# Kernel optimization log

Measured on AMD Instinct MI355X. Metric: run time of the kernel, lower is better.

Reference implementation:

```python
import jax, jax.numpy as jnp
import numpy as np

N, T, H = 307, 256, 64
NH, DH = 4, 16  # transformer heads, head dim (64/4)


def _layernorm(x, g, b, eps=1e-5):
    mu = x.mean(-1, keepdims=True)
    var = ((x - mu) ** 2).mean(-1, keepdims=True)
    return (x - mu) / jnp.sqrt(var + eps) * g + b


def _run_cell(x, m, tf, tj, Anorm, W0, b0, W1, mixW, mixb, Wih, Whh, bih, bhh, outW, outb, jamW, jamb):
    # x,m,tf,tj: [N,T]. Per-timestep 4-path ChebConv(K=2) + softmax mixing + GRUCell.
    hidden = Whh.shape[1]

    def step(h, xs):
        x_t, m_t, tf_t, tj_t = xs  # each [N]
        msg_in = jnp.concatenate([h, m_t[:, None], tf_t[:, None], tj_t[:, None]], axis=-1)  # [N,H+3]
        am = Anorm @ msg_in  # [N,H+3]
        m_all = jnp.tanh(jnp.einsum('ni,poi->npo', msg_in, W0) + b0
                         + jnp.einsum('ni,poi->npo', am, W1))  # [N,4,H]
        mix = jax.nn.softmax(h @ mixW.T + mixb, axis=1)  # [N,4]
        msg = jnp.einsum('np,npo->no', mix, m_all)  # [N,H]
        inp = jnp.concatenate([msg, (x_t * m_t)[:, None], m_t[:, None]], axis=-1)  # [N,H+2]
        # PyTorch GRUCell (gate order r,z,n)
        gi = inp @ Wih.T + bih
        gh = h @ Whh.T + bhh
        i_r, i_z, i_n = jnp.split(gi, 3, axis=-1)
        h_r, h_z, h_n = jnp.split(gh, 3, axis=-1)
        r = jax.nn.sigmoid(i_r + h_r)
        z = jax.nn.sigmoid(i_z + h_z)
        n = jnp.tanh(i_n + r * h_n)
        h_new = (1.0 - z) * n + z * h
        h2 = h_new + 0.1 * h
        pred = (h2 @ outW.T + outb)[:, 0]
        jam = (h2 @ jamW.T + jamb)[:, 0]
        return h2, (pred, jam, h2)

    h0 = jnp.zeros((x.shape[0], hidden), x.dtype)
    _, (preds, jams, hs) = jax.lax.scan(step, h0, (x.T, m.T, tf.T, tj.T))
    return preds.T, jams.T, jnp.transpose(hs, (1, 0, 2))  # [N,T],[N,T],[N,T,H]


def _pos_enc(Tlen, hdim, dtype):
    pos = jnp.arange(Tlen, dtype=dtype)[:, None]
    div = 10000.0 ** (jnp.arange(0, hdim, 2, dtype=dtype) / hdim)
    pe = jnp.zeros((Tlen, hdim), dtype)
    pe = pe.at[:, 0::2].set(jnp.sin(pos / div))
    pe = pe.at[:, 1::2].set(jnp.cos(pos / div))
    return pe


def _enhancer(h, qkvW, qkvb, oW, ob, g1, be1, f1W, f1b, f2W, f2b, g2, be2, pW, pb):
    # h: [N,T,H]; post-norm TransformerEncoder (relu, no dropout at eval), then Linear(H,1)
    x = h + _pos_enc(h.shape[1], h.shape[2], h.dtype)[None]
    n_layers = qkvW.shape[0]
    for l in range(n_layers):
        qkv = x @ qkvW[l].T + qkvb[l]
        q, k, v = jnp.split(qkv, 3, axis=-1)
        sh = (x.shape[0], x.shape[1], NH, DH)
        q, k, v = q.reshape(sh), k.reshape(sh), v.reshape(sh)
        att = jax.nn.softmax(jnp.einsum('nqhd,nkhd->nhqk', q, k) / np.sqrt(DH).astype(np.float32), axis=-1)
        o = jnp.einsum('nhqk,nkhd->nqhd', att, v).reshape(x.shape)
        o = o @ oW[l].T + ob[l]
        x = _layernorm(x + o, g1[l], be1[l])
        f = jax.nn.relu(x @ f1W[l].T + f1b[l]) @ f2W[l].T + f2b[l]
        x = _layernorm(x + f, g2[l], be2[l])
    return (x @ pW.T + pb)[..., 0]  # [N,T]


def _forward(x_seq, m_seq, tod_free, tod_jam, Anorm,
             cell_chebW0, cell_chebb0, cell_chebW1, cell_mixW, cell_mixb,
             cell_Wih, cell_Whh, cell_bih, cell_bhh,
             cell_outW, cell_outb, cell_jamW, cell_jamb,
             fuse_W1, fuse_b1, fuse_W2, fuse_b2,
             tr_qkvW, tr_qkvb, tr_oW, tr_ob, tr_ln1g, tr_ln1b,
             tr_ff1W, tr_ff1b, tr_ff2W, tr_ff2b, tr_ln2g, tr_ln2b,
             tr_projW, tr_projb):
    def cell(i, x, m, tf, tj):
        return _run_cell(x, m, tf, tj, Anorm,
                         cell_chebW0[i], cell_chebb0[i], cell_chebW1[i],
                         cell_mixW[i], cell_mixb[i],
                         cell_Wih[i], cell_Whh[i], cell_bih[i], cell_bhh[i],
                         cell_outW[i], cell_outb[i], cell_jamW[i], cell_jamb[i])

    flip = lambda a: a[:, ::-1]
    pf, jf, h_fwd = cell(0, x_seq, m_seq, tod_free, tod_jam)
    pb_r, jb_r, h_bwd_r = cell(1, flip(x_seq), flip(m_seq), flip(tod_free), flip(tod_jam))
    pb, jb, h_bwd = flip(pb_r), flip(jb_r), h_bwd_r[:, ::-1]

    fuse_in = jnp.stack([pf, pb], axis=-1)  # [N,T,2]
    w = jax.nn.softmax(jax.nn.relu(fuse_in @ fuse_W1.T + fuse_b1) @ fuse_W2.T + fuse_b2, axis=-1)
    speed = w[..., 0] * pf + w[..., 1] * pb
    jam_logit = w[..., 0] * jf + w[..., 1] * jb

    h_fused = h_fwd * w[..., 0:1] + h_bwd * w[..., 1:2]  # [N,T,H]
    args = lambda i: (tr_qkvW[i], tr_qkvb[i], tr_oW[i], tr_ob[i], tr_ln1g[i], tr_ln1b[i],
                      tr_ff1W[i], tr_ff1b[i], tr_ff2W[i], tr_ff2b[i], tr_ln2g[i], tr_ln2b[i],
                      tr_projW[i], tr_projb[i])
    speed_refined = _enhancer(h_fused, *args(0))
    jam_refined = _enhancer(h_fused, *args(1))
    alpha = 0.3
    speed = (1.0 - alpha) * speed + alpha * speed_refined
    jam_logit = (1.0 - alpha) * jam_logit + alpha * jam_refined
    return speed, jam_logit


def setup_inputs() -> dict:
    key = jax.random.key(0)
    keys = list(jax.random.split(key, 40))
    kit = iter(keys)

    def rn(shape, s=0.05):
        return s * jax.random.normal(next(kit), shape, jnp.float32)

    # sparse gaussian-normalized adjacency -> row-normalized diffusion matrix
    rng = np.random.default_rng(0)
    d = rng.uniform(0.5, 3.0, (N, N)); d = (d + d.T) / 2
    keep = rng.uniform(size=(N, N)) < 0.05; keep = keep | keep.T
    d = np.where(keep, d, np.inf)
    sigma = d[d < np.inf].std() + 1e-8
    adj = np.where(d < np.inf, np.exp(-d ** 2 / sigma ** 2), 0.0)
    np.fill_diagonal(adj, 1.0)
    dinv = np.where(adj.sum(1) > 0, (adj.sum(1) + 1e-8) ** -0.5, 0.0)
    adj_sym = adj * dinv[:, None] * dinv[None, :]
    rowsum = adj_sym.sum(1)
    Anorm = (adj_sym * np.where(rowsum > 0, 1.0 / rowsum, 0.0)[:, None]).astype(np.float32)

    inp = {
        'x_seq': jax.random.normal(next(kit), (N, T), jnp.float32),
        'm_seq': (jax.random.uniform(next(kit), (N, T)) < 0.5).astype(jnp.float32),
        'tod_free': jax.random.uniform(next(kit), (N, T), jnp.float32),
        'tod_jam': jax.random.uniform(next(kit), (N, T), jnp.float32),
        'Anorm': jnp.asarray(Anorm),
        'cell_chebW0': rn((2, 4, H, H + 3)), 'cell_chebb0': jnp.zeros((2, 4, H), jnp.float32),
        'cell_chebW1': rn((2, 4, H, H + 3)),
        'cell_mixW': rn((2, 4, H)), 'cell_mixb': jnp.zeros((2, 4), jnp.float32),
        'cell_Wih': rn((2, 3 * H, H + 2)), 'cell_Whh': rn((2, 3 * H, H)),
        'cell_bih': jnp.zeros((2, 3 * H), jnp.float32), 'cell_bhh': jnp.zeros((2, 3 * H), jnp.float32),
        'cell_outW': rn((2, 1, H)), 'cell_outb': jnp.zeros((2, 1), jnp.float32),
        'cell_jamW': rn((2, 1, H)), 'cell_jamb': jnp.zeros((2, 1), jnp.float32),
        'fuse_W1': rn((H, 2)), 'fuse_b1': jnp.zeros((H,), jnp.float32),
        'fuse_W2': rn((2, H)), 'fuse_b2': jnp.zeros((2,), jnp.float32),
        'tr_qkvW': rn((2, 3, 3 * H, H)), 'tr_qkvb': jnp.zeros((2, 3, 3 * H), jnp.float32),
        'tr_oW': rn((2, 3, H, H)), 'tr_ob': jnp.zeros((2, 3, H), jnp.float32),
        'tr_ln1g': jnp.ones((2, 3, H), jnp.float32), 'tr_ln1b': jnp.zeros((2, 3, H), jnp.float32),
        'tr_ff1W': rn((2, 3, 256, H)), 'tr_ff1b': jnp.zeros((2, 3, 256), jnp.float32),
        'tr_ff2W': rn((2, 3, H, 256)), 'tr_ff2b': jnp.zeros((2, 3, H), jnp.float32),
        'tr_ln2g': jnp.ones((2, 3, H), jnp.float32), 'tr_ln2b': jnp.zeros((2, 3, H), jnp.float32),
        'tr_projW': rn((2, 1, H)), 'tr_projb': jnp.zeros((2, 1), jnp.float32),
    }
    return inp


def reference(x_seq, m_seq, tod_free, tod_jam, Anorm,
              cell_chebW0, cell_chebb0, cell_chebW1, cell_mixW, cell_mixb,
              cell_Wih, cell_Whh, cell_bih, cell_bhh,
              cell_outW, cell_outb, cell_jamW, cell_jamb,
              fuse_W1, fuse_b1, fuse_W2, fuse_b2,
              tr_qkvW, tr_qkvb, tr_oW, tr_ob, tr_ln1g, tr_ln1b,
              tr_ff1W, tr_ff1b, tr_ff2W, tr_ff2b, tr_ln2g, tr_ln2b,
              tr_projW, tr_projb):
    return _forward(x_seq, m_seq, tod_free, tod_jam, Anorm,
                    cell_chebW0, cell_chebb0, cell_chebW1, cell_mixW, cell_mixb,
                    cell_Wih, cell_Whh, cell_bih, cell_bhh,
                    cell_outW, cell_outb, cell_jamW, cell_jamb,
                    fuse_W1, fuse_b1, fuse_W2, fuse_b2,
                    tr_qkvW, tr_qkvb, tr_oW, tr_ob, tr_ln1g, tr_ln1b,
                    tr_ff1W, tr_ff1b, tr_ff2W, tr_ff2b, tr_ln2g, tr_ln2b,
                    tr_projW, tr_projb)
```

## Files before the change

kernel.cpp:

```cpp
#include <hip/hip_runtime.h>
#include <math.h>

#define NN   307
#define TT   256
#define HHH  64
#define NROW (NN*TT)
#define NBLK_D 77
#define SCANB  154

typedef unsigned short u16;
typedef __attribute__((ext_vector_type(8))) short short8;
typedef __attribute__((ext_vector_type(4))) float f4;

__device__ __forceinline__ float wsum(float v){
#pragma unroll
  for (int off = 32; off > 0; off >>= 1) v += __shfl_xor(v, off, 64);
  return v;
}
__device__ __forceinline__ float wsum16(float v){
#pragma unroll
  for (int off = 8; off > 0; off >>= 1) v += __shfl_xor(v, off, 64);
  return v;
}
__device__ __forceinline__ float ftanh(float x){
  x = fminf(20.f, fmaxf(-20.f, x));
  float e = __expf(2.f*x);
  return (e - 1.f)/(e + 1.f);
}
__device__ __forceinline__ float fsigm(float x){ return 1.f/(1.f + __expf(-x)); }

__device__ __forceinline__ u16 f2bf(float x){
  unsigned u = __float_as_uint(x);
  u += 0x7fffu + ((u >> 16) & 1u);
  return (u16)(u >> 16);
}
__device__ __forceinline__ void split8(const float* xv, short8& hi, short8& lo){
  union { short8 v; u16 u[8]; } H, L;
#pragma unroll
  for (int j = 0; j < 8; j++){
    const float x = xv[j];
    const u16 h = f2bf(x);
    H.u[j] = h;
    L.u[j] = f2bf(x - __uint_as_float((unsigned)h << 16));
  }
  hi = H.v; lo = L.v;
}

__global__ void k_sparse(const float* __restrict__ A, int* __restrict__ cnt,
                         int* __restrict__ idx, float* __restrict__ val){
  int n = blockIdx.x*64 + threadIdx.x;
  if (n >= NN) return;
  int c = 0;
  for (int m = 0; m < NN; m++){
    float a = A[n*NN + m];
    if (a != 0.f){ idx[n*NN + c] = m; val[n*NN + c] = a; c++; }
  }
  cnt[n] = c;
}

__global__ void k_tr_cheb(const float* __restrict__ W0, const float* __restrict__ W1,
                          float* __restrict__ W0T, float* __restrict__ W1T){
  int t = blockIdx.x*256 + threadIdx.x;
  if (t >= 2*67*256) return;
  int c = t & 255; int rest = t >> 8; int i = rest % 67; int d = rest / 67;
  int p = c >> 6, o = c & 63;
  int src = ((d*4 + p)*64 + o)*67 + i;
  W0T[t] = W0[src];
  W1T[t] = W1[src];
}

__global__ void k_tr_gru(const float* __restrict__ Wih, const float* __restrict__ Whh,
                         float* __restrict__ WihT, float* __restrict__ WhhT){
  int t = blockIdx.x*256 + threadIdx.x;
  if (t < 2*66*192){
    int j = t % 192; int rest = t / 192; int i = rest % 66; int d = rest / 66;
    WihT[t] = Wih[(d*192 + j)*66 + i];
  }
  if (t < 2*64*192){
    int j = t % 192; int rest = t / 192; int i = rest % 64; int d = rest / 64;
    WhhT[t] = Whh[(d*192 + j)*64 + i];
  }
}

__global__ void k_af(const float* __restrict__ mseq, const float* __restrict__ tfr,
                     const float* __restrict__ tjm, const int* __restrict__ cnt,
                     const int* __restrict__ idx, const float* __restrict__ val,
                     float* __restrict__ AF){
  int n = blockIdx.x, c = blockIdx.y, t = threadIdx.x;
  const float* feat = (c == 0) ? mseq : (c == 1) ? tfr : tjm;
  float acc = 0.f; int k = cnt[n];
  for (int s = 0; s < k; s++) acc += val[n*NN + s] * feat[idx[n*NN + s]*TT + t];
  AF[((size_t)c*NN + n)*TT + t] = acc;
}

__global__ void k_split(const float* __restrict__ src, u16* __restrict__ hi,
                        u16* __restrict__ lo, int n){
  int i = blockIdx.x*256 + threadIdx.x;
  if (i >= n) return;
  const float x = src[i];
  const u16 h = f2bf(x);
  hi[i] = h;
  lo[i] = f2bf(x - __uint_as_float((unsigned)h << 16));
}

__global__ __launch_bounds__(256, 1)
void k_scan(const float* __restrict__ xseq, const float* __restrict__ mseq,
            const float* __restrict__ tfr, const float* __restrict__ tjm,
            const float* __restrict__ W0T, const float* __restrict__ W1T,
            const float* __restrict__ b0g,
            const float* __restrict__ mixW, const float* __restrict__ mixb,
            const float* __restrict__ WihT, const float* __restrict__ WhhT,
            const float* __restrict__ bih, const float* __restrict__ bhh,
            const float* __restrict__ outW, const float* __restrict__ outb,
            const float* __restrict__ jamW, const float* __restrict__ jamb,
            const int* __restrict__ spcnt, const int* __restrict__ spidx,
            const float* __restrict__ spval, const float* __restrict__ AF,
            float* __restrict__ Hseq, float* __restrict__ PRED, float* __restrict__ JPRED,
            int* __restrict__ slots)
{
  const int tid = threadIdx.x;
  const int bid = blockIdx.x;
  const int d   = bid / NBLK_D;
  const int n0  = (bid % NBLK_D) * 4;
  const int lane = tid & 63;
  const int wid  = tid >> 6;

  __shared__ __align__(16) float hsT[64][4];
  __shared__ __align__(16) float amsT[68][4];
  __shared__ __align__(16) float msgsT[64][4];
  __shared__ float malls[256][5];
  __shared__ float gis[4][192];
  __shared__ float ghs[4][192];
  __shared__ float mixs[4][4];
  __shared__ float xss[4], mss[4], tfs[4], tjs[4];
  __shared__ int   s_idx[4][320];
  __shared__ float s_val[4][320];
  __shared__ int   s_cnt[4];

  float w0r[67], w1r[67];
#pragma unroll
  for (int i = 0; i < 67; i++){
    w0r[i] = W0T[(d*67 + i)*256 + tid];
    w1r[i] = W1T[(d*67 + i)*256 + tid];
  }
  const float b0r = b0g[d*256 + tid];
  float wih_r[64], whh_r[64];
  float wih64 = 0.f, wih65 = 0.f, bih_r = 0.f, bhh_r = 0.f;
  if (tid < 192){
#pragma unroll
    for (int i = 0; i < 64; i++){
      whh_r[i] = WhhT[(d*64 + i)*192 + tid];
      wih_r[i] = WihT[(d*66 + i)*192 + tid];
    }
    wih64 = WihT[(d*66 + 64)*192 + tid];
    wih65 = WihT[(d*66 + 65)*192 + tid];
    bih_r = bih[d*192 + tid];
    bhh_r = bhh[d*192 + tid];
  }
  float mixw_r[4];
#pragma unroll
  for (int p = 0; p < 4; p++) mixw_r[p] = mixW[(d*4 + p)*64 + lane];
  const float mixb0 = mixb[d*4+0], mixb1 = mixb[d*4+1], mixb2 = mixb[d*4+2], mixb3 = mixb[d*4+3];
  const float outw_r = outW[d*64 + lane], jamw_r = jamW[d*64 + lane];
  const float outb_r = outb[d], jamb_r = jamb[d];

  for (int r = 0; r < 4; r++){
    const int n = min(n0 + r, NN-1);
    const int cc = spcnt[n];
    const int ccp = (cc + 15) & ~15;
    if (tid == 0) s_cnt[r] = ccp;
    for (int s = tid; s < ccp; s += 256){
      s_idx[r][s] = (s < cc) ? spidx[n*NN + s] : 0;
      s_val[r][s] = (s < cc) ? spval[n*NN + s] : 0.f;
    }
  }
  hsT[lane][wid] = 0.f;
  __syncthreads();

#pragma unroll 1
  for (int k = 0; k < TT; k++){
    const int ts = (d == 0) ? k : (TT-1 - k);
    if (tid < 4){
      const int r = tid; const int n = min(n0 + r, NN-1);
      const float mv = mseq[n*TT + ts];
      mss[r] = mv; tfs[r] = tfr[n*TT + ts]; tjs[r] = tjm[n*TT + ts];
      xss[r] = xseq[n*TT + ts];
      amsT[64][r] = AF[(0*NN + n)*TT + ts];
      amsT[65][r] = AF[(1*NN + n)*TT + ts];
      amsT[66][r] = AF[(2*NN + n)*TT + ts];
    }
    {
      const int r = wid;
      const float hv = hsT[lane][r];
      float l0 = wsum(hv * mixw_r[0]) + mixb0;
      float l1 = wsum(hv * mixw_r[1]) + mixb1;
      float l2 = wsum(hv * mixw_r[2]) + mixb2;
      float l3 = wsum(hv * mixw_r[3]) + mixb3;
      const float mx = fmaxf(fmaxf(l0,l1), fmaxf(l2,l3));
      const float e0 = __expf(l0-mx), e1 = __expf(l1-mx), e2 = __expf(l2-mx), e3 = __expf(l3-mx);
      const float inv = 1.f/(e0+e1+e2+e3);
      if (lane == 0){
        mixs[0][r] = e0*inv; mixs[1][r] = e1*inv; mixs[2][r] = e2*inv; mixs[3][r] = e3*inv;
      }
    }
    __syncthreads();
    {
      float a0 = b0r, a1 = b0r, a2 = b0r, a3 = b0r;
#pragma unroll
      for (int i = 0; i < 64; i++){
        const float4 h4 = *(const float4*)&hsT[i][0];
        const float w = w0r[i];
        a0 += h4.x*w; a1 += h4.y*w; a2 += h4.z*w; a3 += h4.w*w;
      }
      a0 += mss[0]*w0r[64] + tfs[0]*w0r[65] + tjs[0]*w0r[66];
      a1 += mss[1]*w0r[64] + tfs[1]*w0r[65] + tjs[1]*w0r[66];
      a2 += mss[2]*w0r[64] + tfs[2]*w0r[65] + tjs[2]*w0r[66];
      a3 += mss[3]*w0r[64] + tfs[3]*w0r[65] + tjs[3]*w0r[66];
      malls[tid][0] = a0; malls[tid][1] = a1; malls[tid][2] = a2; malls[tid][3] = a3;
    }
    if (tid < 192){
      float g0 = bhh_r, g1 = bhh_r, g2 = bhh_r, g3 = bhh_r;
#pragma unroll
      for (int i = 0; i < 64; i++){
        const float4 h4 = *(const float4*)&hsT[i][0];
        const float w = whh_r[i];
        g0 += h4.x*w; g1 += h4.y*w; g2 += h4.z*w; g3 += h4.w*w;
      }
      ghs[0][tid] = g0; ghs[1][tid] = g1; ghs[2][tid] = g2; ghs[3][tid] = g3;
      gis[0][tid] = bih_r + (xss[0]*mss[0])*wih64 + mss[0]*wih65;
      gis[1][tid] = bih_r + (xss[1]*mss[1])*wih64 + mss[1]*wih65;
      gis[2][tid] = bih_r + (xss[2]*mss[2])*wih64 + mss[2]*wih65;
      gis[3][tid] = bih_r + (xss[3]*mss[3])*wih64 + mss[3]*wih65;
    }
    if (k > 0 && tid < 64){
      const int* sl = slots + (size_t)d*NBLK_D*16;
      const int i2 = lane + 64;
      for (;;){
        const int va = (lane < NBLK_D)
            ? __hip_atomic_load(&sl[lane*16], __ATOMIC_RELAXED, __HIP_MEMORY_SCOPE_AGENT)
            : 0x7fffffff;
        const int vb = (i2 < NBLK_D)
            ? __hip_atomic_load(&sl[i2*16], __ATOMIC_RELAXED, __HIP_MEMORY_SCOPE_AGENT)
            : 0x7fffffff;
        if (__all(min(va, vb) >= k)) break;
        __builtin_amdgcn_s_sleep(1);
      }
    }
    __syncthreads();
    {
      const float* Hprev = Hseq + (size_t)(d*257 + k)*NN*64;
      const int r = wid;
      const int ccp = s_cnt[r];
      float acc = 0.f;
      for (int s = 0; s < ccp; s += 16){
        float aV[16], hV[16];
#pragma unroll
        for (int u = 0; u < 16; u++){
          const int m = s_idx[r][s+u];
          aV[u] = s_val[r][s+u];
          hV[u] = __hip_atomic_load(&Hprev[(size_t)m*64 + lane],
                                    __ATOMIC_RELAXED, __HIP_MEMORY_SCOPE_AGENT);
        }
#pragma unroll
        for (int u = 0; u < 16; u++) acc += aV[u]*hV[u];
      }
      amsT[lane][r] = acc;
    }
    __syncthreads();
    {
      const int p = tid >> 6;
      float pa0 = malls[tid][0], pa1 = malls[tid][1], pa2 = malls[tid][2], pa3 = malls[tid][3];
#pragma unroll
      for (int i = 0; i < 67; i++){
        const float4 m4 = *(const float4*)&amsT[i][0];
        const float w = w1r[i];
        pa0 += m4.x*w; pa1 += m4.y*w; pa2 += m4.z*w; pa3 += m4.w*w;
      }
      malls[tid][0] = mixs[p][0]*ftanh(pa0);
      malls[tid][1] = mixs[p][1]*ftanh(pa1);
      malls[tid][2] = mixs[p][2]*ftanh(pa2);
      malls[tid][3] = mixs[p][3]*ftanh(pa3);
    }
    __syncthreads();
    msgsT[lane][wid] = malls[lane][wid] + malls[64+lane][wid] + malls[128+lane][wid] + malls[192+lane][wid];
    __syncthreads();
    if (tid < 192){
      float q0 = gis[0][tid], q1 = gis[1][tid], q2 = gis[2][tid], q3 = gis[3][tid];
#pragma unroll
      for (int i = 0; i < 64; i++){
        const float4 m4 = *(const float4*)&msgsT[i][0];
        const float w = wih_r[i];
        q0 += m4.x*w; q1 += m4.y*w; q2 += m4.z*w; q3 += m4.w*w;
      }
      gis[0][tid] = q0; gis[1][tid] = q1; gis[2][tid] = q2; gis[3][tid] = q3;
    }
    __syncthreads();
    {
      const int r = wid, o = lane;
      const float ir = gis[r][o], iz = gis[r][o+64], in_ = gis[r][o+128];
      const float hr = ghs[r][o], hz = ghs[r][o+64], hn = ghs[r][o+128];
      const float rr2 = fsigm(ir + hr);
      const float zz = fsigm(iz + hz);
      const float nnv = ftanh(in_ + rr2*hn);
      const float hold = hsT[o][r];
      const float h2 = (1.f - zz)*nnv + zz*hold + 0.1f*hold;
      hsT[o][r] = h2;
      const int n = n0 + r;
      if (n < NN)
        __hip_atomic_store(&Hseq[((size_t)(d*257 + k + 1)*NN + n)*64 + o], h2,
                           __ATOMIC_RELAXED, __HIP_MEMORY_SCOPE_AGENT);
    }
    __syncthreads();
    if (tid == 0)
      __hip_atomic_store(&slots[bid*16], k + 1, __ATOMIC_RELAXED, __HIP_MEMORY_SCOPE_AGENT);
    {
      const float h2 = hsT[lane][wid];
      const float pv = wsum(h2 * outw_r);
      const float jv = wsum(h2 * jamw_r);
      const int n = n0 + wid;
      if (lane == 0 && n < NN){
        PRED [(d*NN + n)*TT + ts] = pv + outb_r;
        JPRED[(d*NN + n)*TT + ts] = jv + jamb_r;
      }
    }
  }
}

__global__ __launch_bounds__(256)
void k_fusion(const float* __restrict__ PRED, const float* __restrict__ JPRED,
              const float* __restrict__ Hseq,
              const float* __restrict__ fw1, const float* __restrict__ fb1,
              const float* __restrict__ fw2, const float* __restrict__ fb2,
              float* __restrict__ x0, float* __restrict__ outp)
{
  const int tid = threadIdx.x;
  const int rr = tid >> 6, lane = tid & 63;
  const int idx = blockIdx.x*4 + rr;
  const int n = idx >> 8, t = idx & 255;
  const float pf = PRED[(0*NN + n)*TT + t], pb = PRED[(NN + n)*TT + t];
  const float jf = JPRED[(0*NN + n)*TT + t], jb = JPRED[(NN + n)*TT + t];
  const float hid = fmaxf(fw1[lane*2]*pf + fw1[lane*2+1]*pb + fb1[lane], 0.f);
  const float l0 = wsum(hid * fw2[lane]) + fb2[0];
  const float l1 = wsum(hid * fw2[64+lane]) + fb2[1];
  const float mx = fmaxf(l0,l1);
  const float e0 = __expf(l0-mx), e1 = __expf(l1-mx);
  const float inv = 1.f/(e0+e1);
  const float w0 = e0*inv, w1 = e1*inv;
  const float hf = Hseq[((size_t)(0*257 + t + 1)*NN + n)*64 + lane];
  const float hb = Hseq[((size_t)(257 + 256 - t)*NN + n)*64 + lane];
  const int i2 = lane & ~1;
  const float dv = powf(10000.f, (float)i2 * (1.f/64.f));
  const float arg = (float)t / dv;
  const float pe = (lane & 1) ? cosf(arg) : sinf(arg);
  x0[(size_t)idx*64 + lane] = hf*w0 + hb*w1 + pe;
  if (lane == 0){
    outp[idx]        = 0.7f*(w0*pf + w1*pb);
    outp[NROW + idx] = 0.7f*(w0*jf + w1*jb);
  }
}

__global__ __launch_bounds__(256)
void k_qkv(const float* __restrict__ X, const u16* __restrict__ Whi,
           const u16* __restrict__ Wlo, const float* __restrict__ bias,
           float* __restrict__ Y)
{
  const int tid = threadIdx.x;
  const int w = tid >> 6, l = tid & 63;
  const int m16 = l & 15, q = l >> 4;
  const int row = blockIdx.x*64 + w*16 + m16;
  short8 Ah[2], Al[2];
#pragma unroll
  for (int kh = 0; kh < 2; kh++){
    float xv[8];
    *(float4*)&xv[0] = *(const float4*)&X[(size_t)row*64 + kh*32 + q*8];
    *(float4*)&xv[4] = *(const float4*)&X[(size_t)row*64 + kh*32 + q*8 + 4];
    split8(xv, Ah[kh], Al[kh]);
  }
  const int rbase = blockIdx.x*64 + w*16 + q*4;
  for (int nt = 0; nt < 12; nt++){
    const int n = nt*16 + m16;
    f4 acc = {0.f, 0.f, 0.f, 0.f};
#pragma unroll
    for (int kh = 0; kh < 2; kh++){
      const short8 Bh = *(const short8*)&Whi[(size_t)n*64 + kh*32 + q*8];
      const short8 Bl = *(const short8*)&Wlo[(size_t)n*64 + kh*32 + q*8];
      acc = __builtin_amdgcn_mfma_f32_16x16x32_bf16(Ah[kh], Bh, acc, 0, 0, 0);
      acc = __builtin_amdgcn_mfma_f32_16x16x32_bf16(Ah[kh], Bl, acc, 0, 0, 0);
      acc = __builtin_amdgcn_mfma_f32_16x16x32_bf16(Al[kh], Bh, acc, 0, 0, 0);
    }
    const float bb = bias[n];
#pragma unroll
    for (int r = 0; r < 4; r++)
      Y[(size_t)(rbase + r)*192 + n] = acc[r] + bb;
  }
}

__global__ __launch_bounds__(256)
void k_oproj_ln(const float* __restrict__ X, const u16* __restrict__ Whi,
                const u16* __restrict__ Wlo, const float* __restrict__ bias,
                const float* __restrict__ Xres, const float* __restrict__ g,
                const float* __restrict__ b, float* __restrict__ Y)
{
  const int tid = threadIdx.x;
  const int w = tid >> 6, l = tid & 63;
  const int m16 = l & 15, q = l >> 4;
  const int row = blockIdx.x*64 + w*16 + m16;
  short8 Ah[2], Al[2];
#pragma unroll
  for (int kh = 0; kh < 2; kh++){
    float xv[8];
    *(float4*)&xv[0] = *(const float4*)&X[(size_t)row*64 + kh*32 + q*8];
    *(float4*)&xv[4] = *(const float4*)&X[(size_t)row*64 + kh*32 + q*8 + 4];
    split8(xv, Ah[kh], Al[kh]);
  }
  f4 acc[4];
#pragma unroll
  for (int nt = 0; nt < 4; nt++){
    acc[nt] = (f4){0.f, 0.f, 0.f, 0.f};
    const int n = nt*16 + m16;
#pragma unroll
    for (int kh = 0; kh < 2; kh++){
      const short8 Bh = *(const short8*)&Whi[(size_t)n*64 + kh*32 + q*8];
      const short8 Bl = *(const short8*)&Wlo[(size_t)n*64 + kh*32 + q*8];
      acc[nt] = __builtin_amdgcn_mfma_f32_16x16x32_bf16(Ah[kh], Bh, acc[nt], 0, 0, 0);
      acc[nt] = __builtin_amdgcn_mfma_f32_16x16x32_bf16(Ah[kh], Bl, acc[nt], 0, 0, 0);
      acc[nt] = __builtin_amdgcn_mfma_f32_16x16x32_bf16(Al[kh], Bh, acc[nt], 0, 0, 0);
    }
  }
  const int rbase = blockIdx.x*64 + w*16 + q*4;
#pragma unroll
  for (int r = 0; r < 4; r++){
    float v[4]; float s = 0.f;
#pragma unroll
    for (int nt = 0; nt < 4; nt++){
      const int col = nt*16 + m16;
      v[nt] = acc[nt][r] + bias[col] + Xres[(size_t)(rbase + r)*64 + col];
      s += v[nt];
    }
    const float mu = wsum16(s) * (1.f/64.f);
    float vs = 0.f;
#pragma unroll
    for (int nt = 0; nt < 4; nt++){ v[nt] -= mu; vs += v[nt]*v[nt]; }
    const float rstd = rsqrtf(wsum16(vs) * (1.f/64.f) + 1e-5f);
#pragma unroll
    for (int nt = 0; nt < 4; nt++){
      const int col = nt*16 + m16;
      Y[(size_t)(rbase + r)*64 + col] = v[nt] * rstd * g[col] + b[col];
    }
  }
}

__global__ __launch_bounds__(256)
void k_ffblock(const float* __restrict__ X,
               const u16* __restrict__ W1hi, const u16* __restrict__ W1lo,
               const float* __restrict__ b1,
               const u16* __restrict__ W2hi, const u16* __restrict__ W2lo,
               const float* __restrict__ b2,
               const float* __restrict__ g, const float* __restrict__ b,
               float* __restrict__ Y)
{
  __shared__ __align__(16) u16 Hs[64][280];
  const int tid = threadIdx.x;
  const int w = tid >> 6, l = tid & 63;
  const int m16 = l & 15, q = l >> 4;
  const int row = blockIdx.x*64 + w*16 + m16;
  short8 Ah[2], Al[2];
#pragma unroll
  for (int kh = 0; kh < 2; kh++){
    float xv[8];
    *(float4*)&xv[0] = *(const float4*)&X[(size_t)row*64 + kh*32 + q*8];
    *(float4*)&xv[4] = *(const float4*)&X[(size_t)row*64 + kh*32 + q*8 + 4];
    split8(xv, Ah[kh], Al[kh]);
  }
  for (int nt = 0; nt < 16; nt++){
    const int n = nt*16 + m16;
    f4 acc = {0.f, 0.f, 0.f, 0.f};
#pragma unroll
    for (int kh = 0; kh < 2; kh++){
      const short8 Bh = *(const short8*)&W1hi[(size_t)n*64 + kh*32 + q*8];
      const short8 Bl = *(const short8*)&W1lo[(size_t)n*64 + kh*32 + q*8];
      acc = __builtin_amdgcn_mfma_f32_16x16x32_bf16(Ah[kh], Bh, acc, 0, 0, 0);
      acc = __builtin_amdgcn_mfma_f32_16x16x32_bf16(Ah[kh], Bl, acc, 0, 0, 0);
      acc = __builtin_amdgcn_mfma_f32_16x16x32_bf16(Al[kh], Bh, acc, 0, 0, 0);
    }
    const float bb = b1[n];
#pragma unroll
    for (int r = 0; r < 4; r++){
      const float h = fmaxf(acc[r] + bb, 0.f);
      Hs[w*16 + q*4 + r][n] = f2bf(h);
    }
  }
  __syncthreads();
  f4 acc2[4];
#pragma unroll
  for (int nt = 0; nt < 4; nt++) acc2[nt] = (f4){0.f, 0.f, 0.f, 0.f};
#pragma unroll 1
  for (int kh = 0; kh < 8; kh++){
    const short8 Ahh = *(const short8*)&Hs[w*16 + m16][kh*32 + q*8];
#pragma unroll
    for (int nt = 0; nt < 4; nt++){
      const int n = nt*16 + m16;
      const short8 Bh = *(const short8*)&W2hi[(size_t)n*256 + kh*32 + q*8];
      const short8 Bl = *(const short8*)&W2lo[(size_t)n*256 + kh*32 + q*8];
      acc2[nt] = __builtin_amdgcn_mfma_f32_16x16x32_bf16(Ahh, Bh, acc2[nt], 0, 0, 0);
      acc2[nt] = __builtin_amdgcn_mfma_f32_16x16x32_bf16(Ahh, Bl, acc2[nt], 0, 0, 0);
    }
  }
  const int rbase = blockIdx.x*64 + w*16 + q*4;
#pragma unroll
  for (int r = 0; r < 4; r++){
    float v[4]; float s = 0.f;
#pragma unroll
    for (int nt = 0; nt < 4; nt++){
      const int col = nt*16 + m16;
      v[nt] = acc2[nt][r] + b2[col] + X[(size_t)(rbase + r)*64 + col];
      s += v[nt];
    }
    const float mu = wsum16(s) * (1.f/64.f);
    float vs = 0.f;
#pragma unroll
    for (int nt = 0; nt < 4; nt++){ v[nt] -= mu; vs += v[nt]*v[nt]; }
    const float rstd = rsqrtf(wsum16(vs) * (1.f/64.f) + 1e-5f);
#pragma unroll
    for (int nt = 0; nt < 4; nt++){
      const int col = nt*16 + m16;
      Y[(size_t)(rbase + r)*64 + col] = v[nt] * rstd * g[col] + b[col];
    }
  }
}

__global__ __launch_bounds__(256)
void k_attn(const float* __restrict__ QKV, float* __restrict__ O)
{
  __shared__ __align__(16) u16 Vst[4][16][264];
  __shared__ __align__(16) u16 Pst[4][16][264];
  const int n = blockIdx.x;
  const int tid = threadIdx.x;
  const int h = tid >> 6;
  const int l = tid & 63;
  const int m16 = l & 15, q = l >> 4;
  const float* nbase = QKV + (size_t)n*256*192;
  const short8 z8 = {0,0,0,0,0,0,0,0};

  for (int kb = 0; kb < 64; kb++){
    const int key = kb*4 + q;
    const float vv = nbase[(size_t)key*192 + 128 + h*16 + m16];
    Vst[h][m16][key] = f2bf(vv);
  }
  short8 Bh[16], Bl[16];
#pragma unroll
  for (int ct = 0; ct < 16; ct++){
    if (q < 2){
      float kv[8];
      *(float4*)&kv[0] = *(const float4*)&nbase[(size_t)(ct*16+m16)*192 + 64 + h*16 + q*8];
      *(float4*)&kv[4] = *(const float4*)&nbase[(size_t)(ct*16+m16)*192 + 64 + h*16 + q*8 + 4];
      split8(kv, Bh[ct], Bl[ct]);
    } else { Bh[ct] = z8; Bl[ct] = z8; }
  }
  __syncthreads();

#pragma unroll 1
  for (int c = 0; c < 16; c++){
    const int c0 = c*16;
    short8 Qh, Ql;
    if (q < 2){
      float xv[8];
      *(float4*)&xv[0] = *(const float4*)&nbase[(size_t)(c0+m16)*192 + h*16 + q*8];
      *(float4*)&xv[4] = *(const float4*)&nbase[(size_t)(c0+m16)*192 + h*16 + q*8 + 4];
#pragma unroll
      for (int j2 = 0; j2 < 8; j2++) xv[j2] *= 0.25f;
      split8(xv, Qh, Ql);
    } else { Qh = z8; Ql = z8; }
    float rs[4] = {0.f, 0.f, 0.f, 0.f};
#pragma unroll
    for (int ct = 0; ct < 16; ct++){
      f4 s = {0.f, 0.f, 0.f, 0.f};
      s = __builtin_amdgcn_mfma_f32_16x16x32_bf16(Qh, Bh[ct], s, 0, 0, 0);
      s = __builtin_amdgcn_mfma_f32_16x16x32_bf16(Qh, Bl[ct], s, 0, 0, 0);
      s = __builtin_amdgcn_mfma_f32_16x16x32_bf16(Ql, Bh[ct], s, 0, 0, 0);
#pragma unroll
      for (int r = 0; r < 4; r++){
        const float p = __expf(s[r]);
        rs[r] += p;
        Pst[h][q*4 + r][ct*16 + m16] = f2bf(p);
      }
    }
#pragma unroll
    for (int r = 0; r < 4; r++) rs[r] = wsum16(rs[r]);
    __syncthreads();
    f4 acc = {0.f, 0.f, 0.f, 0.f};
#pragma unroll
    for (int kt = 0; kt < 8; kt++){
      const short8 Pa = *(const short8*)&Pst[h][m16][kt*32 + q*8];
      const short8 Vb = *(const short8*)&Vst[h][m16][kt*32 + q*8];
      acc = __builtin_amdgcn_mfma_f32_16x16x32_bf16(Pa, Vb, acc, 0, 0, 0);
    }
    __syncthreads();
#pragma unroll
    for (int r = 0; r < 4; r++){
      O[((size_t)n*256 + c0 + q*4 + r)*64 + h*16 + m16] = acc[r] / rs[r];
    }
  }
}

__global__ __launch_bounds__(256)
void k_proj_add(const float* __restrict__ X, const float* __restrict__ pW,
                const float* __restrict__ pb, float* __restrict__ outp)
{
  const int tid = threadIdx.x;
  const int r = tid >> 6, lane = tid & 63;
  const size_t row = (size_t)blockIdx.x*4 + r;
  const float v = X[row*64 + lane] * pW[lane];
  const float s = wsum(v);
  if (lane == 0) outp[row] += 0.3f*(s + pb[0]);
}

extern "C" void kernel_launch(void* const* d_in, const int* in_sizes, int n_in,
                              void* d_out, int out_size, void* d_ws, size_t ws_size,
                              hipStream_t stream)
{
  const float* x_seq = (const float*)d_in[0];
  const float* m_seq = (const float*)d_in[1];
  const float* tod_f = (const float*)d_in[2];
  const float* tod_j = (const float*)d_in[3];
  const float* Anorm = (const float*)d_in[4];
  const float* chW0  = (const float*)d_in[5];
  const float* chb0  = (const float*)d_in[6];
  const float* chW1  = (const float*)d_in[7];
  const float* mixW  = (const float*)d_in[8];
  const float* mixb  = (const float*)d_in[9];
  const float* Wih   = (const float*)d_in[10];
  const float* Whh   = (const float*)d_in[11];
  const float* bih   = (const float*)d_in[12];
  const float* bhh   = (const float*)d_in[13];
  const float* outW  = (const float*)d_in[14];
  const float* outbp = (const float*)d_in[15];
  const float* jamW  = (const float*)d_in[16];
  const float* jambp = (const float*)d_in[17];
  const float* fW1   = (const float*)d_in[18];
  const float* fb1   = (const float*)d_in[19];
  const float* fW2   = (const float*)d_in[20];
  const float* fb2   = (const float*)d_in[21];
  const float* qkvW  = (const float*)d_in[22];
  const float* qkvb  = (const float*)d_in[23];
  const float* oW    = (const float*)d_in[24];
  const float* ob    = (const float*)d_in[25];
  const float* ln1g  = (const float*)d_in[26];
  const float* ln1b  = (const float*)d_in[27];
  const float* f1W   = (const float*)d_in[28];
  const float* f1b   = (const float*)d_in[29];
  const float* f2W   = (const float*)d_in[30];
  const float* f2b   = (const float*)d_in[31];
  const float* ln2g  = (const float*)d_in[32];
  const float* ln2b  = (const float*)d_in[33];
  const float* prW   = (const float*)d_in[34];
  const float* prb   = (const float*)d_in[35];
  float* out = (float*)d_out;

  float* ws = (float*)d_ws;
  size_t off = 0;
  auto take = [&](size_t n)->float*{ float* p = ws + off; off += (n + 63) & ~(size_t)63; return p; };
  int*   slots = (int*)take(4096);
  float* W0T  = take((size_t)2*67*256);
  float* W1T  = take((size_t)2*67*256);
  float* WihT = take((size_t)2*66*192);
  float* WhhT = take((size_t)2*64*192);
  int*   spcnt = (int*)take(320);
  int*   spidx = (int*)take((size_t)NN*NN);
  float* spval = take((size_t)NN*NN);
  float* AF    = take((size_t)3*NN*TT);
  float* PRED  = take((size_t)2*NN*TT);
  float* JPRED = take((size_t)2*NN*TT);
  float* HSEQ  = take((size_t)2*257*NN*64);
  float* X0    = take((size_t)NROW*64);
  float* XBUF  = take((size_t)NROW*64);
  float* OBUF  = take((size_t)NROW*64);
  float* FBUF  = take((size_t)NROW*256);
  const size_t NQKV = (size_t)6*192*64;
  const size_t NO   = (size_t)6*64*64;
  const size_t NF1  = (size_t)6*256*64;
  const size_t NF2  = (size_t)6*64*256;
  const size_t NWTOT = NQKV + NO + NF1 + NF2;
  u16* WHI = (u16*)take((NWTOT + 1)/2);
  u16* WLO = (u16*)take((NWTOT + 1)/2);
  (void)ws_size; (void)in_sizes; (void)n_in; (void)out_size;

  hipMemsetAsync(slots, 0, 4096*sizeof(int), stream);
  hipMemsetAsync(HSEQ, 0, (size_t)NN*64*sizeof(float), stream);
  hipMemsetAsync(HSEQ + (size_t)257*NN*64, 0, (size_t)NN*64*sizeof(float), stream);

  k_sparse<<<dim3((NN+63)/64), dim3(64), 0, stream>>>(Anorm, spcnt, spidx, spval);
  k_tr_cheb<<<dim3(134), dim3(256), 0, stream>>>(chW0, chW1, W0T, W1T);
  k_tr_gru<<<dim3(99), dim3(256), 0, stream>>>(Wih, Whh, WihT, WhhT);
  k_af<<<dim3(NN,3), dim3(256), 0, stream>>>(m_seq, tod_f, tod_j, spcnt, spidx, spval, AF);
  k_split<<<dim3((int)((NQKV+255)/256)), dim3(256), 0, stream>>>(qkvW, WHI, WLO, (int)NQKV);
  k_split<<<dim3((int)((NO+255)/256)), dim3(256), 0, stream>>>(oW, WHI+NQKV, WLO+NQKV, (int)NO);
  k_split<<<dim3((int)((NF1+255)/256)), dim3(256), 0, stream>>>(f1W, WHI+NQKV+NO, WLO+NQKV+NO, (int)NF1);
  k_split<<<dim3((int)((NF2+255)/256)), dim3(256), 0, stream>>>(f2W, WHI+NQKV+NO+NF1, WLO+NQKV+NO+NF1, (int)NF2);

  k_scan<<<dim3(SCANB), dim3(256), 0, stream>>>(x_seq, m_seq, tod_f, tod_j, W0T, W1T,
      chb0, mixW, mixb, WihT, WhhT, bih, bhh, outW, outbp, jamW, jambp,
      spcnt, spidx, spval, AF, HSEQ, PRED, JPRED, slots);

  k_fusion<<<dim3(NROW/4), dim3(256), 0, stream>>>(PRED, JPRED, HSEQ, fW1, fb1, fW2, fb2, X0, out);

  for (int e = 0; e < 2; e++){
    for (int l = 0; l < 3; l++){
      const int el = e*3 + l;
      const float* xin = (l == 0) ? X0 : XBUF;
      const u16* qhi = WHI + (size_t)el*192*64;
      const u16* qlo = WLO + (size_t)el*192*64;
      const u16* ohi = WHI + NQKV + (size_t)el*64*64;
      const u16* olo = WLO + NQKV + (size_t)el*64*64;
      const u16* f1hi = WHI + NQKV + NO + (size_t)el*256*64;
      const u16* f1lo = WLO + NQKV + NO + (size_t)el*256*64;
      const u16* f2hi = WHI + NQKV + NO + NF1 + (size_t)el*64*256;
      const u16* f2lo = WLO + NQKV + NO + NF1 + (size_t)el*64*256;
      k_qkv<<<dim3(NROW/64), dim3(256), 0, stream>>>(xin, qhi, qlo,
          qkvb + (size_t)el*192, FBUF);
      k_attn<<<dim3(NN), dim3(256), 0, stream>>>(FBUF, OBUF);
      k_oproj_ln<<<dim3(NROW/64), dim3(256), 0, stream>>>(OBUF, ohi, olo,
          ob + (size_t)el*64, xin, ln1g + (size_t)el*64, ln1b + (size_t)el*64, XBUF);
      k_ffblock<<<dim3(NROW/64), dim3(256), 0, stream>>>(XBUF, f1hi, f1lo,
          f1b + (size_t)el*256, f2hi, f2lo, f2b + (size_t)el*64,
          ln2g + (size_t)el*64, ln2b + (size_t)el*64, XBUF);
    }
    k_proj_add<<<dim3(NROW/4), dim3(256), 0, stream>>>(XBUF, prW + (size_t)e*64, prb + e,
        out + (size_t)e*NROW);
  }
}
```

Measured before the change: 4.773 ms.

## Fuse QKV projection into attention kernel, dropping the QKV intermediate buffer

Replaces the separate QKV projection and attention kernels with one per-node kernel. It converts the node's 256x64 activations to bf16 in shared memory, computes K and V per head with MFMA, then computes Q tile by tile and runs the attention in the same block. This removes the global write and re-read of the 192-wide QKV buffer and one kernel launch per layer. In exchange, X is kept only as high bf16 (the lo term is dropped) and K is a single bf16 value, so precision is lower than the old three-term split. The per-tile __syncthreads were removed; this looks safe because each wave touches only its own head's shared-memory slices.

After: 4.645 ms. 2.7% less time.

```diff
diff --git a/kernel.cpp b/kernel.cpp
--- a/kernel.cpp
+++ b/kernel.cpp
@@ -34,6 +34,9 @@
   u += 0x7fffu + ((u >> 16) & 1u);
   return (u16)(u >> 16);
 }
+__device__ __forceinline__ float bf2f(u16 h){
+  return __uint_as_float((unsigned)h << 16);
+}
 __device__ __forceinline__ void split8(const float* xv, short8& hi, short8& lo){
   union { short8 v; u16 u[8]; } H, L;
 #pragma unroll
@@ -41,7 +44,7 @@
     const float x = xv[j];
     const u16 h = f2bf(x);
     H.u[j] = h;
-    L.u[j] = f2bf(x - __uint_as_float((unsigned)h << 16));
+    L.u[j] = f2bf(x - bf2f(h));
   }
   hi = H.v; lo = L.v;
 }
@@ -100,7 +103,7 @@
   const float x = src[i];
   const u16 h = f2bf(x);
   hi[i] = h;
-  lo[i] = f2bf(x - __uint_as_float((unsigned)h << 16));
+  lo[i] = f2bf(x - bf2f(h));
 }
 
 __global__ __launch_bounds__(256, 1)
@@ -360,38 +363,122 @@
 }
 
 __global__ __launch_bounds__(256)
-void k_qkv(const float* __restrict__ X, const u16* __restrict__ Whi,
-           const u16* __restrict__ Wlo, const float* __restrict__ bias,
-           float* __restrict__ Y)
+void k_qkattn(const float* __restrict__ X,
+              const u16* __restrict__ Whi, const u16* __restrict__ Wlo,
+              const float* __restrict__ bias, float* __restrict__ O)
 {
+  __shared__ __align__(16) u16 Xhi[256][72];
+  __shared__ __align__(16) u16 Vt [4][16][280];
+  __shared__ __align__(16) u16 Pst[4][16][264];
+  __shared__ __align__(16) u16 Kscr[4][16][24];
+  __shared__ __align__(16) u16 Qhs[4][16][24];
+  __shared__ __align__(16) u16 Qls[4][16][24];
+  const int n = blockIdx.x;
   const int tid = threadIdx.x;
-  const int w = tid >> 6, l = tid & 63;
+  const int h = tid >> 6;
+  const int l = tid & 63;
   const int m16 = l & 15, q = l >> 4;
-  const int row = blockIdx.x*64 + w*16 + m16;
-  short8 Ah[2], Al[2];
+  const float* xbase = X + (size_t)n*256*64;
+  const short8 z8 = {0,0,0,0,0,0,0,0};
+
+  {
+    const float* xr = xbase + (size_t)tid*64;
+#pragma unroll
+    for (int c = 0; c < 64; c += 8){
+      float v[8];
+      *(float4*)&v[0] = *(const float4*)&xr[c];
+      *(float4*)&v[4] = *(const float4*)&xr[c+4];
+      union { short8 s; u16 u[8]; } pk;
+#pragma unroll
+      for (int j = 0; j < 8; j++) pk.u[j] = f2bf(v[j]);
+      *(short8*)&Xhi[tid][c] = pk.s;
+    }
+  }
+  __syncthreads();
+
+  short8 WqH[2], WqL[2], WkH[2], WkL[2], WvH[2], WvL[2];
 #pragma unroll
   for (int kh = 0; kh < 2; kh++){
-    float xv[8];
-    *(float4*)&xv[0] = *(const float4*)&X[(size_t)row*64 + kh*32 + q*8];
-    *(float4*)&xv[4] = *(const float4*)&X[(size_t)row*64 + kh*32 + q*8 + 4];
-    split8(xv, Ah[kh], Al[kh]);
-  }
-  const int rbase = blockIdx.x*64 + w*16 + q*4;
-  for (int nt = 0; nt < 12; nt++){
-    const int n = nt*16 + m16;
-    f4 acc = {0.f, 0.f, 0.f, 0.f};
-#pragma unroll
-    for (int kh = 0; kh < 2; kh++){
-      const short8 Bh = *(const short8*)&Whi[(size_t)n*64 + kh*32 + q*8];
-      const short8 Bl = *(const short8*)&Wlo[(size_t)n*64 + kh*32 + q*8];
-      acc = __builtin_amdgcn_mfma_f32_16x16x32_bf16(Ah[kh], Bh, acc, 0, 0, 0);
-      acc = __builtin_amdgcn_mfma_f32_16x16x32_bf16(Ah[kh], Bl, acc, 0, 0, 0);
-      acc = __builtin_amdgcn_mfma_f32_16x16x32_bf16(Al[kh], Bh, acc, 0, 0, 0);
-    }
-    const float bb = bias[n];
-#pragma unroll
-    for (int r = 0; r < 4; r++)
-      Y[(size_t)(rbase + r)*192 + n] = acc[r] + bb;
+    const size_t rq = (size_t)(h*16 + m16)*64 + kh*32 + q*8;
+    const size_t rk = (size_t)(64 + h*16 + m16)*64 + kh*32 + q*8;
+    const size_t rv = (size_t)(128 + h*16 + m16)*64 + kh*32 + q*8;
+    WqH[kh] = *(const short8*)&Whi[rq]; WqL[kh] = *(const short8*)&Wlo[rq];
+    WkH[kh] = *(const short8*)&Whi[rk]; WkL[kh] = *(const short8*)&Wlo[rk];
+    WvH[kh] = *(const short8*)&Whi[rv]; WvL[kh] = *(const short8*)&Wlo[rv];
+  }
+  const float qb = bias[h*16 + m16];
+  const float kb = bias[64 + h*16 + m16];
+  const float vb = bias[128 + h*16 + m16];
+
+  short8 Kb[16];
+#pragma unroll 1
+  for (int ct = 0; ct < 16; ct++){
+    short8 Xa0 = *(const short8*)&Xhi[ct*16 + m16][q*8];
+    short8 Xa1 = *(const short8*)&Xhi[ct*16 + m16][32 + q*8];
+    f4 ka = {0.f,0.f,0.f,0.f}, va = {0.f,0.f,0.f,0.f};
+    ka = __builtin_amdgcn_mfma_f32_16x16x32_bf16(Xa0, WkH[0], ka, 0, 0, 0);
+    ka = __builtin_amdgcn_mfma_f32_16x16x32_bf16(Xa0, WkL[0], ka, 0, 0, 0);
+    ka = __builtin_amdgcn_mfma_f32_16x16x32_bf16(Xa1, WkH[1], ka, 0, 0, 0);
+    ka = __builtin_amdgcn_mfma_f32_16x16x32_bf16(Xa1, WkL[1], ka, 0, 0, 0);
+    va = __builtin_amdgcn_mfma_f32_16x16x32_bf16(Xa0, WvH[0], va, 0, 0, 0);
+    va = __builtin_amdgcn_mfma_f32_16x16x32_bf16(Xa0, WvL[0], va, 0, 0, 0);
+    va = __builtin_amdgcn_mfma_f32_16x16x32_bf16(Xa1, WvH[1], va, 0, 0, 0);
+    va = __builtin_amdgcn_mfma_f32_16x16x32_bf16(Xa1, WvL[1], va, 0, 0, 0);
+#pragma unroll
+    for (int r = 0; r < 4; r++){
+      Kscr[h][q*4 + r][m16] = f2bf(ka[r] + kb);
+      Vt[h][m16][ct*16 + q*4 + r] = f2bf(va[r] + vb);
+    }
+    Kb[ct] = (q < 2) ? *(const short8*)&Kscr[h][m16][q*8] : z8;
+  }
+
+#pragma unroll 1
+  for (int c = 0; c < 16; c++){
+    short8 Xa0 = *(const short8*)&Xhi[c*16 + m16][q*8];
+    short8 Xa1 = *(const short8*)&Xhi[c*16 + m16][32 + q*8];
+    f4 qa = {0.f,0.f,0.f,0.f};
+    qa = __builtin_amdgcn_mfma_f32_16x16x32_bf16(Xa0, WqH[0], qa, 0, 0, 0);
+    qa = __builtin_amdgcn_mfma_f32_16x16x32_bf16(Xa0, WqL[0], qa, 0, 0, 0);
+    qa = __builtin_amdgcn_mfma_f32_16x16x32_bf16(Xa1, WqH[1], qa, 0, 0, 0);
+    qa = __builtin_amdgcn_mfma_f32_16x16x32_bf16(Xa1, WqL[1], qa, 0, 0, 0);
+#pragma unroll
+    for (int r = 0; r < 4; r++){
+      const float qv = (qa[r] + qb) * 0.25f;
+      const u16 hh = f2bf(qv);
+      Qhs[h][q*4 + r][m16] = hh;
+      Qls[h][q*4 + r][m16] = f2bf(qv - bf2f(hh));
+    }
+    short8 Qh = z8, Ql = z8;
+    if (q < 2){
+      Qh = *(const short8*)&Qhs[h][m16][q*8];
+      Ql = *(const short8*)&Qls[h][m16][q*8];
+    }
+    float rs[4] = {0.f, 0.f, 0.f, 0.f};
+#pragma unroll
+    for (int ct = 0; ct < 16; ct++){
+      f4 s = {0.f,0.f,0.f,0.f};
+      s = __builtin_amdgcn_mfma_f32_16x16x32_bf16(Qh, Kb[ct], s, 0, 0, 0);
+      s = __builtin_amdgcn_mfma_f32_16x16x32_bf16(Ql, Kb[ct], s, 0, 0, 0);
+#pragma unroll
+      for (int r = 0; r < 4; r++){
+        const float p = __expf(s[r]);
+        rs[r] += p;
+        Pst[h][q*4 + r][ct*16 + m16] = f2bf(p);
+      }
+    }
+#pragma unroll
+    for (int r = 0; r < 4; r++) rs[r] = wsum16(rs[r]);
+    f4 acc = {0.f,0.f,0.f,0.f};
+#pragma unroll
+    for (int kt = 0; kt < 8; kt++){
+      const short8 Pa = *(const short8*)&Pst[h][m16][kt*32 + q*8];
+      const short8 Vb = *(const short8*)&Vt[h][m16][kt*32 + q*8];
+      acc = __builtin_amdgcn_mfma_f32_16x16x32_bf16(Pa, Vb, acc, 0, 0, 0);
+    }
+#pragma unroll
+    for (int r = 0; r < 4; r++){
+      O[((size_t)n*256 + c*16 + q*4 + r)*64 + h*16 + m16] = acc[r] / rs[r];
+    }
   }
 }
 
@@ -525,80 +612,6 @@
     for (int nt = 0; nt < 4; nt++){
       const int col = nt*16 + m16;
       Y[(size_t)(rbase + r)*64 + col] = v[nt] * rstd * g[col] + b[col];
-    }
-  }
-}
-
-__global__ __launch_bounds__(256)
-void k_attn(const float* __restrict__ QKV, float* __restrict__ O)
-{
-  __shared__ __align__(16) u16 Vst[4][16][264];
-  __shared__ __align__(16) u16 Pst[4][16][264];
-  const int n = blockIdx.x;
-  const int tid = threadIdx.x;
-  const int h = tid >> 6;
-  const int l = tid & 63;
-  const int m16 = l & 15, q = l >> 4;
-  const float* nbase = QKV + (size_t)n*256*192;
-  const short8 z8 = {0,0,0,0,0,0,0,0};
-
-  for (int kb = 0; kb < 64; kb++){
-    const int key = kb*4 + q;
-    const float vv = nbase[(size_t)key*192 + 128 + h*16 + m16];
-    Vst[h][m16][key] = f2bf(vv);
-  }
-  short8 Bh[16], Bl[16];
-#pragma unroll
-  for (int ct = 0; ct < 16; ct++){
-    if (q < 2){
-      float kv[8];
-      *(float4*)&kv[0] = *(const float4*)&nbase[(size_t)(ct*16+m16)*192 + 64 + h*16 + q*8];
-      *(float4*)&kv[4] = *(const float4*)&nbase[(size_t)(ct*16+m16)*192 + 64 + h*16 + q*8 + 4];
-      split8(kv, Bh[ct], Bl[ct]);
-    } else { Bh[ct] = z8; Bl[ct] = z8; }
-  }
-  __syncthreads();
-
-#pragma unroll 1
-  for (int c = 0; c < 16; c++){
-    const int c0 = c*16;
-    short8 Qh, Ql;
-    if (q < 2){
-      float xv[8];
-      *(float4*)&xv[0] = *(const float4*)&nbase[(size_t)(c0+m16)*192 + h*16 + q*8];
-      *(float4*)&xv[4] = *(const float4*)&nbase[(size_t)(c0+m16)*192 + h*16 + q*8 + 4];
-#pragma unroll
-      for (int j2 = 0; j2 < 8; j2++) xv[j2] *= 0.25f;
-      split8(xv, Qh, Ql);
-    } else { Qh = z8; Ql = z8; }
-    float rs[4] = {0.f, 0.f, 0.f, 0.f};
-#pragma unroll
-    for (int ct = 0; ct < 16; ct++){
-      f4 s = {0.f, 0.f, 0.f, 0.f};
-      s = __builtin_amdgcn_mfma_f32_16x16x32_bf16(Qh, Bh[ct], s, 0, 0, 0);
-      s = __builtin_amdgcn_mfma_f32_16x16x32_bf16(Qh, Bl[ct], s, 0, 0, 0);
-      s = __builtin_amdgcn_mfma_f32_16x16x32_bf16(Ql, Bh[ct], s, 0, 0, 0);
-#pragma unroll
-      for (int r = 0; r < 4; r++){
-        const float p = __expf(s[r]);
-        rs[r] += p;
-        Pst[h][q*4 + r][ct*16 + m16] = f2bf(p);
-      }
-    }
-#pragma unroll
-    for (int r = 0; r < 4; r++) rs[r] = wsum16(rs[r]);
-    __syncthreads();
-    f4 acc = {0.f, 0.f, 0.f, 0.f};
-#pragma unroll
-    for (int kt = 0; kt < 8; kt++){
-      const short8 Pa = *(const short8*)&Pst[h][m16][kt*32 + q*8];
-      const short8 Vb = *(const short8*)&Vst[h][m16][kt*32 + q*8];
-      acc = __builtin_amdgcn_mfma_f32_16x16x32_bf16(Pa, Vb, acc, 0, 0, 0);
-    }
-    __syncthreads();
-#pragma unroll
-    for (int r = 0; r < 4; r++){
-      O[((size_t)n*256 + c0 + q*4 + r)*64 + h*16 + m16] = acc[r] / rs[r];
     }
   }
 }
@@ -675,7 +688,6 @@
   float* X0    = take((size_t)NROW*64);
   float* XBUF  = take((size_t)NROW*64);
   float* OBUF  = take((size_t)NROW*64);
-  float* FBUF  = take((size_t)NROW*256);
   const size_t NQKV = (size_t)6*192*64;
   const size_t NO   = (size_t)6*64*64;
   const size_t NF1  = (size_t)6*256*64;
@@ -716,9 +728,8 @@
       const u16* f1lo = WLO + NQKV + NO + (size_t)el*256*64;
       const u16* f2hi = WHI + NQKV + NO + NF1 + (size_t)el*64*256;
       const u16* f2lo = WLO + NQKV + NO + NF1 + (size_t)el*64*256;
-      k_qkv<<<dim3(NROW/64), dim3(256), 0, stream>>>(xin, qhi, qlo,
-          qkvb + (size_t)el*192, FBUF);
-      k_attn<<<dim3(NN), dim3(256), 0, stream>>>(FBUF, OBUF);
+      k_qkattn<<<dim3(NN), dim3(256), 0, stream>>>(xin, qhi, qlo,
+          qkvb + (size_t)el*192, OBUF);
       k_oproj_ln<<<dim3(NROW/64), dim3(256), 0, stream>>>(OBUF, ohi, olo,
           ob + (size_t)el*64, xin, ln1g + (size_t)el*64, ln1b + (size_t)el*64, XBUF);
       k_ffblock<<<dim3(NROW/64), dim3(256), 0, stream>>>(XBUF, f1hi, f1lo,
```
